# Optimization experiments

Measured on AMD Instinct MI355X. Metric: run time of the kernel, lower is better.

Reference implementation:

```python
import jax, jax.numpy as jnp
import numpy as np

B, S, D, H = 2, 2048, 1024, 16
HD = D // H  # 64


def setup_inputs() -> dict:
    key = jax.random.key(0)
    ks = jax.random.split(key, 5)
    sc = 1.0 / np.sqrt(D)
    return {
        "x": jax.random.normal(ks[0], (B, S, D), jnp.float32),
        "wq": jax.random.normal(ks[1], (D, D), jnp.float32) * sc,
        "bq": jnp.zeros((D,), jnp.float32),
        "wk": jax.random.normal(ks[2], (D, D), jnp.float32) * sc,
        "bk": jnp.zeros((D,), jnp.float32),
        "wv": jax.random.normal(ks[3], (D, D), jnp.float32) * sc,
        "bv": jnp.zeros((D,), jnp.float32),
        "wo": jax.random.normal(ks[4], (D, D), jnp.float32) * sc,
        "bo": jnp.zeros((D,), jnp.float32),
    }


def _rope_tables(seq_len, dim):
    inv_freq = 1.0 / (10000.0 ** (jnp.arange(0, dim, 2, dtype=jnp.float32) / dim))
    t = jnp.arange(seq_len, dtype=jnp.float32)
    freqs = jnp.einsum("i,j->ij", t, inv_freq)  # [S, dim/2]
    emb = jnp.concatenate([freqs, freqs], axis=-1)  # [S, dim]
    return jnp.cos(emb)[None, None], jnp.sin(emb)[None, None]  # [1,1,S,dim]


def _rotate_half(x):
    x1, x2 = x[..., : x.shape[-1] // 2], x[..., x.shape[-1] // 2 :]
    return jnp.concatenate([-x2, x1], axis=-1)


def reference(x, wq, bq, wk, bk, wv, bv, wo, bo):
    b, s, d = x.shape
    h, hd = H, d // H
    # projections (torch Linear: x @ W.T + b) -> [b, h, s, hd]
    def proj(w, bias):
        return (x @ w.T + bias).reshape(b, s, h, hd).transpose(0, 2, 1, 3)

    q, k, v = proj(wq, bq), proj(wk, bk), proj(wv, bv)
    cos, sin = _rope_tables(s, hd)
    q = q * cos + _rotate_half(q) * sin
    k = k * cos + _rotate_half(k) * sin
    scores = jnp.einsum("bhqd,bhkd->bhqk", q, k) / jnp.sqrt(jnp.float32(hd))
    attn = jax.nn.softmax(scores, axis=-1)
    out = jnp.einsum("bhqk,bhkd->bhqd", attn, v)
    out = out.transpose(0, 2, 1, 3).reshape(b, s, d)
    return out @ wo.T + bo
```

## Files before the change

kernel.cpp:

```cpp
#include <hip/hip_runtime.h>
#include <hip/hip_bf16.h>

#define Bq 2
#define Sq 2048
#define Dq 1024
#define Hq 16
#define QSCALE 0.18033688011112042f

typedef __attribute__((ext_vector_type(8))) short short8;
typedef __attribute__((ext_vector_type(4))) float floatx4;
typedef unsigned short ushort_t;

#define VMCNT0() asm volatile("s_waitcnt vmcnt(0)" ::: "memory")
#define GLDS(src, dst) __builtin_amdgcn_global_load_lds( \
    (const __attribute__((address_space(1))) void*)(src), \
    (__attribute__((address_space(3))) void*)(dst), 16, 0, 0)

__device__ __forceinline__ ushort_t f2bf(float f) {
    union { float f; unsigned u; } v; v.f = f;
    unsigned u = v.u;
    u += 0x7fffu + ((u >> 16) & 1u);
    return (ushort_t)(u >> 16);
}

__device__ __forceinline__ unsigned pk_bf16(float a, float b) {
    union { __hip_bfloat162 h; unsigned u; } c;
    c.h = __float22bfloat162_rn(float2{a, b});
    return c.u;
}

__device__ __forceinline__ void cvt8(const float* __restrict__ in, ushort_t* __restrict__ out, int i) {
    const float4* p = (const float4*)in + (size_t)i * 2;
    float4 a = p[0], b = p[1];
    ushort4 lo, hi;
    lo.x = f2bf(a.x); lo.y = f2bf(a.y); lo.z = f2bf(a.z); lo.w = f2bf(a.w);
    hi.x = f2bf(b.x); hi.y = f2bf(b.y); hi.z = f2bf(b.z); hi.w = f2bf(b.w);
    *(ushort4*)(out + (size_t)i * 8)     = lo;
    *(ushort4*)(out + (size_t)i * 8 + 4) = hi;
}

__global__ void prep(const float* __restrict__ x,
                     const float* __restrict__ wq, const float* __restrict__ wk,
                     const float* __restrict__ wv, const float* __restrict__ wo,
                     ushort_t* __restrict__ xb,
                     ushort_t* __restrict__ wqb, ushort_t* __restrict__ wkb,
                     ushort_t* __restrict__ wvb, ushort_t* __restrict__ wob,
                     float* __restrict__ cost, float* __restrict__ sint) {
    int b = blockIdx.x;
    if (b < 2048) {
        cvt8(x, xb, b * 256 + threadIdx.x);
    } else if (b < 4096) {
        int w = (b - 2048) >> 9;
        int i = ((b - 2048) & 511) * 256 + threadIdx.x;
        const float* src = (w == 0) ? wq : (w == 1) ? wk : (w == 2) ? wv : wo;
        ushort_t* dst    = (w == 0) ? wqb : (w == 1) ? wkb : (w == 2) ? wvb : wob;
        cvt8(src, dst, i);
    } else {
        int i = (b - 4096) * 256 + threadIdx.x;
        int s = i >> 5, f = i & 31;
        float invf = powf(10000.0f, -(float)f / 32.0f);
        float ang = (float)s * invf;
        cost[i] = cosf(ang);
        sint[i] = sinf(ang);
    }
}

__global__ __launch_bounds__(256, 3) void gemm_qkv(
    const ushort_t* __restrict__ xb,
    const ushort_t* __restrict__ wqb, const ushort_t* __restrict__ wkb, const ushort_t* __restrict__ wvb,
    const float* __restrict__ bq, const float* __restrict__ bk, const float* __restrict__ bv,
    const float* __restrict__ cost, const float* __restrict__ sint,
    ushort_t* __restrict__ qout, ushort_t* __restrict__ kout, ushort_t* __restrict__ vtout)
{
    __shared__ ushort_t As0[128 * 32], As1[128 * 32];
    __shared__ ushort_t Bs0[128 * 32], Bs1[128 * 32];
    const int mode = blockIdx.z;
    const ushort_t* W  = (mode == 0) ? wqb : (mode == 1) ? wkb : wvb;
    const float* bias  = (mode == 0) ? bq  : (mode == 1) ? bk  : bv;

    const int t = threadIdx.x;
    const int lane = t & 63;
    const int wid = t >> 6;
    const int l15 = lane & 15, lk = lane >> 4;
    const int wr = wid >> 1, wc = wid & 1;
    const int rowBase = blockIdx.y * 128;
    const int colBase = blockIdx.x * 128;

    floatx4 acc[4][4] = {};

    const char* aSrc[2];
    const char* bSrc[2];
    int ldso[2];
#pragma unroll
    for (int issue = 0; issue < 2; ++issue) {
        int ldsoff = issue * 4096 + t * 16;
        int row = ldsoff >> 6;
        int cb  = ldsoff & 63;
        ldso[issue] = ldsoff;
        aSrc[issue] = (const char*)xb + (size_t)(rowBase + row) * 2048 + cb;
        bSrc[issue] = (const char*)W  + (size_t)(colBase + row) * 2048 + cb;
    }

    auto STAGE = [&](ushort_t* Ad, ushort_t* Bd) {
#pragma unroll
        for (int issue = 0; issue < 2; ++issue) {
            GLDS(aSrc[issue], (char*)Ad + ldso[issue]);
            GLDS(bSrc[issue], (char*)Bd + ldso[issue]);
        }
        aSrc[0] += 64; aSrc[1] += 64; bSrc[0] += 64; bSrc[1] += 64;
    };

    auto KSTEP = [&](const ushort_t* Ac, const ushort_t* Bc, int knext, ushort_t* An, ushort_t* Bn) {
        if (knext < Dq) STAGE(An, Bn);
        short8 a[4], b[4];
#pragma unroll
        for (int m = 0; m < 4; ++m)
            a[m] = *(const short8*)((const char*)Ac + (wr * 64 + m * 16 + l15) * 64 + lk * 16);
#pragma unroll
        for (int n = 0; n < 4; ++n)
            b[n] = *(const short8*)((const char*)Bc + (wc * 64 + n * 16 + l15) * 64 + lk * 16);
        __builtin_amdgcn_s_setprio(1);
#pragma unroll
        for (int m = 0; m < 4; ++m)
#pragma unroll
            for (int n = 0; n < 4; ++n)
                acc[m][n] = __builtin_amdgcn_mfma_f32_16x16x32_bf16(a[m], b[n], acc[m][n], 0, 0, 0);
        __builtin_amdgcn_s_setprio(0);
        VMCNT0();
        __syncthreads();
    };

    STAGE(As0, Bs0);
    VMCNT0();
    __syncthreads();

#pragma unroll 1
    for (int k0 = 0; k0 < Dq; k0 += 64) {
        KSTEP(As0, Bs0, k0 + 32, As1, Bs1);
        KSTEP(As1, Bs1, k0 + 64, As0, Bs0);
    }

    const int colW = colBase + wc * 64;
    const int hh = colW >> 6;

    if (mode < 2) {
        ushort_t* outp = (mode == 0) ? qout : kout;
        const float osc = (mode == 0) ? QSCALE : 1.0f;
#pragma unroll
        for (int m = 0; m < 4; ++m) {
            int rg0 = rowBase + wr * 64 + m * 16 + lk * 4;
#pragma unroll
            for (int n2 = 0; n2 < 2; ++n2) {
                int d0 = n2 * 16 + l15;
                float b0 = bias[colW + d0];
                float b2 = bias[colW + d0 + 32];
#pragma unroll
                for (int r = 0; r < 4; ++r) {
                    int rg = rg0 + r;
                    int bb = rg >> 11;
                    int s  = rg & 2047;
                    float c  = cost[s * 32 + d0];
                    float sn = sint[s * 32 + d0];
                    float a0 = acc[m][n2][r]     + b0;
                    float a2 = acc[m][n2 + 2][r] + b2;
                    float o0 = (a0 * c - a2 * sn) * osc;
                    float o2 = (a2 * c + a0 * sn) * osc;
                    size_t base = ((size_t)(bb * Hq + hh) * Sq + s) * 64;
                    outp[base + d0]      = f2bf(o0);
                    outp[base + d0 + 32] = f2bf(o2);
                }
            }
        }
    } else {
#pragma unroll
        for (int m = 0; m < 4; ++m) {
            int rg0 = rowBase + wr * 64 + m * 16 + lk * 4;
            int bb  = rg0 >> 11;
            int s0  = rg0 & 2047;
            int g   = (s0 & 63) >> 2;
            int ng  = (g >> 3) * 8 + (g & 3) * 2 + ((g >> 2) & 1);
            int s2b = (s0 & ~63) + ng * 4;
#pragma unroll
            for (int n = 0; n < 4; ++n) {
                int d = n * 16 + l15;
                float bb_ = bias[colW + d];
#pragma unroll
                for (int r = 0; r < 4; ++r)
                    vtout[((size_t)(bb * Hq + hh) * 64 + d) * Sq + s2b + r] = f2bf(acc[m][n][r] + bb_);
            }
        }
    }
}

__global__ __launch_bounds__(256, 4) void flash_attn(
    const ushort_t* __restrict__ qbuf, const ushort_t* __restrict__ kbuf,
    const ushort_t* __restrict__ vtbuf, ushort_t* __restrict__ abuf)
{
    __shared__ char Ks0[64 * 128], Ks1[64 * 128];
    __shared__ char Vs0[64 * 128], Vs1[64 * 128];

    const int t = threadIdx.x, lane = t & 63, wid = t >> 6;
    const int l15 = lane & 15, lk = lane >> 4;

    int flat = blockIdx.y * 32 + blockIdx.x;
    flat = (flat & 7) * 128 + (flat >> 3);
    const int qtile = flat & 31, bh = flat >> 5;
    const int bpos = bh >> 4, h = bh & 15;
    const int qbase = qtile * 64 + wid * 16;

    const ushort_t* Qp = qbuf + ((size_t)bh * Sq + qbase) * 64;
    short8 qf[2];
#pragma unroll
    for (int kk = 0; kk < 2; ++kk)
        qf[kk] = *(const short8*)(Qp + l15 * 64 + kk * 32 + lk * 8);

    short8 onesf;
#pragma unroll
    for (int j = 0; j < 8; ++j) onesf[j] = (short)0x3F80;

    floatx4 oacc[4] = {};
    floatx4 lacc = {};
    float mrow = -INFINITY;

    int off_[4][2];
#pragma unroll
    for (int n = 0; n < 4; ++n) {
        int swz = (l15 & 7) << 4;
#pragma unroll
        for (int kk = 0; kk < 2; ++kk)
            off_[n][kk] = (n * 16 + l15) * 128 + ((kk * 64 + lk * 16) ^ swz);
    }

    const char* Kg = (const char*)kbuf  + (size_t)bh * Sq * 128;
    const char* Vg = (const char*)vtbuf + (size_t)bh * 64 * Sq * 2;
    unsigned kOff[2], vOff[2];
    int ldso[2];
#pragma unroll
    for (int issue = 0; issue < 2; ++issue) {
        int ldsoff = issue * 4096 + t * 16;
        int row = ldsoff >> 7;
        int pb  = ldsoff & 127;
        int lb  = pb ^ ((row & 7) << 4);
        ldso[issue] = ldsoff;
        kOff[issue] = (unsigned)(row * 128 + lb);
        vOff[issue] = (unsigned)(row * 4096 + lb);
    }

    auto STAGE = [&](char* Kd, char* Vd) {
#pragma unroll
        for (int issue = 0; issue < 2; ++issue) {
            GLDS(Kg + kOff[issue], Kd + ldso[issue]);
            GLDS(Vg + vOff[issue], Vd + ldso[issue]);
        }
        kOff[0] += 8192; kOff[1] += 8192; vOff[0] += 128; vOff[1] += 128;
    };

    auto TILE = [&](const char* Kc, const char* Vc, int kvnext, char* Kn, char* Vn) {
        if (kvnext < Sq) STAGE(Kn, Vn);

        short8 kf[4][2];
#pragma unroll
        for (int n = 0; n < 4; ++n)
#pragma unroll
            for (int kk = 0; kk < 2; ++kk)
                kf[n][kk] = *(const short8*)(Kc + off_[n][kk]);

        floatx4 sacc[4] = {};
        __builtin_amdgcn_s_setprio(1);
#pragma unroll
        for (int kk = 0; kk < 2; ++kk)
#pragma unroll
            for (int n = 0; n < 4; ++n)
                sacc[n] = __builtin_amdgcn_mfma_f32_16x16x32_bf16(kf[n][kk], qf[kk], sacc[n], 0, 0, 0);
        __builtin_amdgcn_s_setprio(0);

        short8 vf[4][2];
#pragma unroll
        for (int n = 0; n < 4; ++n)
#pragma unroll
            for (int kb = 0; kb < 2; ++kb)
                vf[n][kb] = *(const short8*)(Vc + off_[n][kb]);

        float part = fmaxf(fmaxf(sacc[0][0], sacc[0][1]), sacc[0][2]);
        part = fmaxf(fmaxf(part, sacc[0][3]), sacc[1][0]);
        part = fmaxf(fmaxf(part, sacc[1][1]), sacc[1][2]);
        part = fmaxf(fmaxf(part, sacc[1][3]), sacc[2][0]);
        part = fmaxf(fmaxf(part, sacc[2][1]), sacc[2][2]);
        part = fmaxf(fmaxf(part, sacc[2][3]), sacc[3][0]);
        part = fmaxf(fmaxf(part, sacc[3][1]), sacc[3][2]);
        part = fmaxf(part, sacc[3][3]);

        if (!__all(part - mrow <= 8.0f)) {
            float pmax = part;
            pmax = fmaxf(pmax, __shfl_xor(pmax, 16));
            pmax = fmaxf(pmax, __shfl_xor(pmax, 32));
            float mnew = fmaxf(mrow, pmax);
            float corr = __builtin_exp2f(mrow - mnew);
            mrow = mnew;
#pragma unroll
            for (int r = 0; r < 4; ++r) {
                float c = __shfl(corr, (lane & 48) | (lk * 4 + r));
                lacc[r] *= c;
#pragma unroll
                for (int n = 0; n < 4; ++n) oacc[n][r] *= c;
            }
        }

        float p[4][4];
#pragma unroll
        for (int n = 0; n < 4; ++n)
#pragma unroll
            for (int r = 0; r < 4; ++r)
                p[n][r] = __builtin_exp2f(sacc[n][r] - mrow);

        short8 paf[2];
#pragma unroll
        for (int kb = 0; kb < 2; ++kb) {
            union { unsigned u[4]; short8 v; } pu;
            pu.u[0] = pk_bf16(p[2 * kb][0],     p[2 * kb][1]);
            pu.u[1] = pk_bf16(p[2 * kb][2],     p[2 * kb][3]);
            pu.u[2] = pk_bf16(p[2 * kb + 1][0], p[2 * kb + 1][1]);
            pu.u[3] = pk_bf16(p[2 * kb + 1][2], p[2 * kb + 1][3]);
            paf[kb] = pu.v;
        }

        __builtin_amdgcn_s_setprio(1);
#pragma unroll
        for (int kb = 0; kb < 2; ++kb) {
#pragma unroll
            for (int n = 0; n < 4; ++n)
                oacc[n] = __builtin_amdgcn_mfma_f32_16x16x32_bf16(paf[kb], vf[n][kb], oacc[n], 0, 0, 0);
            lacc = __builtin_amdgcn_mfma_f32_16x16x32_bf16(paf[kb], onesf, lacc, 0, 0, 0);
        }
        __builtin_amdgcn_s_setprio(0);

        VMCNT0();
        __syncthreads();
    };

    STAGE(Ks0, Vs0);
    VMCNT0();
    __syncthreads();

#pragma unroll 1
    for (int kv0 = 0; kv0 < Sq; kv0 += 128) {
        TILE(Ks0, Vs0, kv0 + 64,  Ks1, Vs1);
        TILE(Ks1, Vs1, kv0 + 128, Ks0, Vs0);
    }

#pragma unroll
    for (int r = 0; r < 4; ++r) {
        float linv = 1.0f / lacc[r];
        int srow = qbase + lk * 4 + r;
        size_t base = ((size_t)bpos * Sq + srow) * Dq + h * 64;
#pragma unroll
        for (int n = 0; n < 4; ++n)
            abuf[base + n * 16 + l15] = f2bf(oacc[n][r] * linv);
    }
}

__global__ __launch_bounds__(256, 4) void gemm_out(
    const ushort_t* __restrict__ ab, const ushort_t* __restrict__ wob,
    const float* __restrict__ bo, float* __restrict__ out)
{
    __shared__ ushort_t As0[128 * 32], As1[128 * 32];
    __shared__ ushort_t Bs0[64 * 32],  Bs1[64 * 32];
    const int t = threadIdx.x;
    const int lane = t & 63;
    const int wid = t >> 6;
    const int l15 = lane & 15, lk = lane >> 4;
    const int wr = wid >> 1, wc = wid & 1;
    const int rowBase = blockIdx.y * 128;
    const int colBase = blockIdx.x * 64;

    floatx4 acc[4][2] = {};

    const char* aSrc[2];
    const char* bSrc;
    int ldso[2];
#pragma unroll
    for (int issue = 0; issue < 2; ++issue) {
        int ldsoff = issue * 4096 + t * 16;
        int row = ldsoff >> 6;
        int cb  = ldsoff & 63;
        ldso[issue] = ldsoff;
        aSrc[issue] = (const char*)ab + (size_t)(rowBase + row) * 2048 + cb;
    }
    {
        int ldsoff = t * 16;
        int row = ldsoff >> 6;
        int cb  = ldsoff & 63;
        bSrc = (const char*)wob + (size_t)(colBase + row) * 2048 + cb;
    }

    auto STAGE = [&](ushort_t* Ad, ushort_t* Bd) {
#pragma unroll
        for (int issue = 0; issue < 2; ++issue)
            GLDS(aSrc[issue], (char*)Ad + ldso[issue]);
        GLDS(bSrc, (char*)Bd + ldso[0]);
        aSrc[0] += 64; aSrc[1] += 64; bSrc += 64;
    };

    auto KSTEP = [&](const ushort_t* Ac, const ushort_t* Bc, int knext, ushort_t* An, ushort_t* Bn) {
        if (knext < Dq) STAGE(An, Bn);
        short8 a[4], b[2];
#pragma unroll
        for (int m = 0; m < 4; ++m)
            a[m] = *(const short8*)((const char*)Ac + (wr * 64 + m * 16 + l15) * 64 + lk * 16);
#pragma unroll
        for (int n = 0; n < 2; ++n)
            b[n] = *(const short8*)((const char*)Bc + (wc * 32 + n * 16 + l15) * 64 + lk * 16);
        __builtin_amdgcn_s_setprio(1);
#pragma unroll
        for (int m = 0; m < 4; ++m)
#pragma unroll
            for (int n = 0; n < 2; ++n)
                acc[m][n] = __builtin_amdgcn_mfma_f32_16x16x32_bf16(a[m], b[n], acc[m][n], 0, 0, 0);
        __builtin_amdgcn_s_setprio(0);
        VMCNT0();
        __syncthreads();
    };

    STAGE(As0, Bs0);
    VMCNT0();
    __syncthreads();

#pragma unroll 1
    for (int k0 = 0; k0 < Dq; k0 += 64) {
        KSTEP(As0, Bs0, k0 + 32, As1, Bs1);
        KSTEP(As1, Bs1, k0 + 64, As0, Bs0);
    }

    const int colW = colBase + wc * 32;
#pragma unroll
    for (int m = 0; m < 4; ++m) {
        int rg0 = rowBase + wr * 64 + m * 16 + lk * 4;
#pragma unroll
        for (int n = 0; n < 2; ++n) {
            int colg = colW + n * 16 + l15;
            float bb_ = bo[colg];
#pragma unroll
            for (int r = 0; r < 4; ++r)
                out[(size_t)(rg0 + r) * Dq + colg] = acc[m][n][r] + bb_;
        }
    }
}

extern "C" void kernel_launch(void* const* d_in, const int* in_sizes, int n_in,
                              void* d_out, int out_size, void* d_ws, size_t ws_size,
                              hipStream_t stream) {
    (void)in_sizes; (void)n_in; (void)out_size;
    const float* x  = (const float*)d_in[0];
    const float* wq = (const float*)d_in[1];
    const float* bq = (const float*)d_in[2];
    const float* wk = (const float*)d_in[3];
    const float* bk = (const float*)d_in[4];
    const float* wv = (const float*)d_in[5];
    const float* bv = (const float*)d_in[6];
    const float* wo = (const float*)d_in[7];
    const float* bo = (const float*)d_in[8];
    float* out = (float*)d_out;

    if (ws_size < 50855936) return;
    char* ws = (char*)d_ws;
    ushort_t* xb   = (ushort_t*)(ws + 0);
    ushort_t* wqb  = (ushort_t*)(ws + 8388608);
    ushort_t* wkb  = (ushort_t*)(ws + 10485760);
    ushort_t* wvb  = (ushort_t*)(ws + 12582912);
    ushort_t* wob  = (ushort_t*)(ws + 14680064);
    ushort_t* qb   = (ushort_t*)(ws + 16777216);
    ushort_t* kb   = (ushort_t*)(ws + 25165824);
    ushort_t* vtb  = (ushort_t*)(ws + 33554432);
    ushort_t* abuf = (ushort_t*)(ws + 41943040);
    float*    cost = (float*)(ws + 50331648);
    float*    sint = (float*)(ws + 50593792);

    prep<<<4352, 256, 0, stream>>>(x, wq, wk, wv, wo, xb, wqb, wkb, wvb, wob, cost, sint);
    gemm_qkv<<<dim3(8, 32, 3), 256, 0, stream>>>(xb, wqb, wkb, wvb, bq, bk, bv, cost, sint, qb, kb, vtb);
    flash_attn<<<dim3(32, 32), 256, 0, stream>>>(qb, kb, vtb, abuf);
    gemm_out<<<dim3(16, 32), 256, 0, stream>>>(abuf, wob, bo, out);
}
```

Baseline: 125.8 us.

## Software-pipeline flash attention so PV of previous tile overlaps QK of next

Restructures the attention loop so the P·V MFMAs for the previous KV tile are issued alongside the Q·K MFMAs of the current tile. The probabilities and V fragments are carried in registers across iterations, with a prologue tile and an epilogue PV step. The intent is to hide the softmax/exp latency between dependent MFMA groups. Because the carried registers raise register pressure, the launch-bounds occupancy hint drops from 4 to 3 blocks per CU, which may reduce latency hiding across waves.

```diff
diff --git a/kernel.cpp b/kernel.cpp
--- a/kernel.cpp
+++ b/kernel.cpp
@@ -192,7 +192,7 @@
     }
 }
 
-__global__ __launch_bounds__(256, 4) void flash_attn(
+__global__ __launch_bounds__(256, 3) void flash_attn(
     const ushort_t* __restrict__ qbuf, const ushort_t* __restrict__ kbuf,
     const ushort_t* __restrict__ vtbuf, ushort_t* __restrict__ abuf)
 {
@@ -221,6 +221,9 @@
     floatx4 oacc[4] = {};
     floatx4 lacc = {};
     float mrow = -INFINITY;
+
+    short8 pafp[2];
+    short8 vfp[4][2];
 
     int off_[4][2];
 #pragma unroll
@@ -255,8 +258,8 @@
         kOff[0] += 8192; kOff[1] += 8192; vOff[0] += 128; vOff[1] += 128;
     };
 
-    auto TILE = [&](const char* Kc, const char* Vc, int kvnext, char* Kn, char* Vn) {
-        if (kvnext < Sq) STAGE(Kn, Vn);
+    auto TILEP = [&](const char* Kc, const char* Vc, bool doStage, char* Kn, char* Vn, bool doPV) {
+        if (doStage) STAGE(Kn, Vn);
 
         short8 kf[4][2];
 #pragma unroll
@@ -272,14 +275,22 @@
 #pragma unroll
             for (int n = 0; n < 4; ++n)
                 sacc[n] = __builtin_amdgcn_mfma_f32_16x16x32_bf16(kf[n][kk], qf[kk], sacc[n], 0, 0, 0);
+        if (doPV) {
+#pragma unroll
+            for (int kb = 0; kb < 2; ++kb) {
+#pragma unroll
+                for (int n = 0; n < 4; ++n)
+                    oacc[n] = __builtin_amdgcn_mfma_f32_16x16x32_bf16(pafp[kb], vfp[n][kb], oacc[n], 0, 0, 0);
+                lacc = __builtin_amdgcn_mfma_f32_16x16x32_bf16(pafp[kb], onesf, lacc, 0, 0, 0);
+            }
+        }
         __builtin_amdgcn_s_setprio(0);
 
-        short8 vf[4][2];
 #pragma unroll
         for (int n = 0; n < 4; ++n)
 #pragma unroll
             for (int kb = 0; kb < 2; ++kb)
-                vf[n][kb] = *(const short8*)(Vc + off_[n][kb]);
+                vfp[n][kb] = *(const short8*)(Vc + off_[n][kb]);
 
         float part = fmaxf(fmaxf(sacc[0][0], sacc[0][1]), sacc[0][2]);
         part = fmaxf(fmaxf(part, sacc[0][3]), sacc[1][0]);
@@ -313,7 +324,6 @@
             for (int r = 0; r < 4; ++r)
                 p[n][r] = __builtin_exp2f(sacc[n][r] - mrow);
 
-        short8 paf[2];
 #pragma unroll
         for (int kb = 0; kb < 2; ++kb) {
             union { unsigned u[4]; short8 v; } pu;
@@ -321,18 +331,8 @@
             pu.u[1] = pk_bf16(p[2 * kb][2],     p[2 * kb][3]);
             pu.u[2] = pk_bf16(p[2 * kb + 1][0], p[2 * kb + 1][1]);
             pu.u[3] = pk_bf16(p[2 * kb + 1][2], p[2 * kb + 1][3]);
-            paf[kb] = pu.v;
-        }
-
-        __builtin_amdgcn_s_setprio(1);
-#pragma unroll
-        for (int kb = 0; kb < 2; ++kb) {
-#pragma unroll
-            for (int n = 0; n < 4; ++n)
-                oacc[n] = __builtin_amdgcn_mfma_f32_16x16x32_bf16(paf[kb], vf[n][kb], oacc[n], 0, 0, 0);
-            lacc = __builtin_amdgcn_mfma_f32_16x16x32_bf16(paf[kb], onesf, lacc, 0, 0, 0);
-        }
-        __builtin_amdgcn_s_setprio(0);
+            pafp[kb] = pu.v;
+        }
 
         VMCNT0();
         __syncthreads();
@@ -342,11 +342,25 @@
     VMCNT0();
     __syncthreads();
 
+    TILEP(Ks0, Vs0, true, Ks1, Vs1, false);
+
 #pragma unroll 1
-    for (int kv0 = 0; kv0 < Sq; kv0 += 128) {
-        TILE(Ks0, Vs0, kv0 + 64,  Ks1, Vs1);
-        TILE(Ks1, Vs1, kv0 + 128, Ks0, Vs0);
-    }
+    for (int i = 0; i < 15; ++i) {
+        TILEP(Ks1, Vs1, true, Ks0, Vs0, true);
+        TILEP(Ks0, Vs0, true, Ks1, Vs1, true);
+    }
+
+    TILEP(Ks1, Vs1, false, Ks0, Vs0, true);
+
+    __builtin_amdgcn_s_setprio(1);
+#pragma unroll
+    for (int kb = 0; kb < 2; ++kb) {
+#pragma unroll
+        for (int n = 0; n < 4; ++n)
+            oacc[n] = __builtin_amdgcn_mfma_f32_16x16x32_bf16(pafp[kb], vfp[n][kb], oacc[n], 0, 0, 0);
+        lacc = __builtin_amdgcn_mfma_f32_16x16x32_bf16(pafp[kb], onesf, lacc, 0, 0, 0);
+    }
+    __builtin_amdgcn_s_setprio(0);
 
 #pragma unroll
     for (int r = 0; r < 4; ++r) {
```

Measured after the change: 127.9 us. No clear change (+1.6%).
